# Performance work log

Measured on AMD Instinct MI355X. Metric: run time of the kernel, lower is better.

## Reference

```python
import jax, jax.numpy as jnp
import numpy as np

B, W, L, J, I, O = 512, 1024, 64, 8, 32, 128


def setup_inputs() -> dict:
    key = jax.random.key(0)
    ks = jax.random.split(key, 9)
    wm = jax.random.normal(ks[0], (B, W, L), dtype=jnp.float32)
    constants = jax.random.uniform(ks[1], (J, L), minval=-1.0, maxval=1.0, dtype=jnp.float32)
    gammas = jax.random.uniform(ks[2], (J, L), minval=0.0, maxval=1.0, dtype=jnp.float32)
    body_w = jax.random.normal(ks[3], (J, I, L), dtype=jnp.float32) / np.sqrt(L).astype(np.float32)
    body_b = jax.random.normal(ks[4], (J, I), dtype=jnp.float32) * 0.01
    slot_w = jax.random.normal(ks[5], (J, L * I, L), dtype=jnp.float32) / np.sqrt(L).astype(np.float32)
    slot_b = jax.random.normal(ks[6], (J, L * I), dtype=jnp.float32) * 0.01
    head_w = jax.random.normal(ks[7], (O, I), dtype=jnp.float32) / np.sqrt(I).astype(np.float32)
    head_b = jax.random.normal(ks[8], (O,), dtype=jnp.float32) * 0.01
    return {"working_memory": wm, "constants": constants, "gammas": gammas,
            "body_w": body_w, "body_b": body_b, "slot_w": slot_w, "slot_b": slot_b,
            "head_w": head_w, "head_b": head_b}


def reference(working_memory, constants, gammas, body_w, body_b, slot_w, slot_b, head_w, head_b):
    temperature = 1.0
    g = jnp.clip(gammas, 0.0, 1.0)            # (J,L), torch.clamp equivalent
    w1 = 1.0 - g                               # per-element weight (1-gamma)
    # match_scores[j,b,w] = sum_l w1[j,l] * (c[j,l] - wm[b,w,l])^2, expanded to
    # avoid materializing a (J,B,W,L) intermediate:
    A = jnp.sum(w1 * constants * constants, axis=1)                      # (J,)
    cross = jnp.einsum('jl,bwl->jbw', w1 * constants, working_memory)    # (J,B,W)
    quad = jnp.einsum('jl,bwl->jbw', w1, working_memory * working_memory)
    scores = A[:, None, None] - 2.0 * cross + quad                       # (J,B,W)
    attn = jax.nn.softmax(-scores / temperature, axis=-1)                # (J,B,W)
    best = jnp.einsum('jbw,bwl->jbl', attn, working_memory)              # (J,B,L)
    total_mq = jnp.sum(attn * scores, axis=-1).sum(axis=0)               # (B,)
    # body: per-premise Linear(L->I), scaled by mean clamped gamma
    captured = jnp.einsum('jbl,jil->jbi', best, body_w) + body_b[:, None, :]
    g_avg = g.mean(axis=1)                                               # (J,)
    captured_vars = jnp.einsum('j,jbi->bi', g_avg, captured)             # (B,I)
    # slot selector: per-premise Linear(L -> L*I), softmax over slots,
    # scatter best_props values into slots (the original inner l-loop).
    slot_logits = jnp.einsum('jbl,jkl->jbk', best, slot_w) + slot_b[:, None, :]
    slot_probs = jax.nn.softmax(slot_logits.reshape(J, -1, L, I), axis=-1)
    captured_vars = captured_vars + jnp.einsum('jbli,jbl->bi', slot_probs, best)
    output = captured_vars @ head_w.T + head_b                           # (B,O)
    confidence = jnp.exp(-total_mq)[:, None]                             # (B,1)
    return confidence * output
```

## Files before the change

### kernel.cpp

```cpp
#include <hip/hip_runtime.h>
#include <cstdint>
#include <cstddef>

#define B_ 512
#define W_ 1024
#define L_ 64
#define J_ 8
#define I_ 32
#define O_ 128


typedef const __attribute__((address_space(1))) void* gas_ptr;
typedef __attribute__((address_space(3))) void* las_ptr;

__global__ __launch_bounds__(64) void k0_prep(const float* __restrict__ constants,
    const float* __restrict__ gammas, float* __restrict__ wcg,
    float* __restrict__ w1g, float* __restrict__ Ag)
{
  const int l = threadIdx.x;
  #pragma unroll
  for (int j = 0; j < J_; ++j) {
    float g = gammas[j*L_ + l];
    g = fminf(fmaxf(g, 0.f), 1.f);
    float c = constants[j*L_ + l];
    float w1 = 1.f - g;
    w1g[j*L_ + l] = w1;
    wcg[j*L_ + l] = -2.f * w1 * c;
  }
  if (l < J_) {
    float a = 0.f;
    for (int c = 0; c < L_; ++c) {
      float g = gammas[l*L_ + c];
      g = fminf(fmaxf(g, 0.f), 1.f);
      float cc = constants[l*L_ + c];
      a += (1.f - g) * cc * cc;
    }
    Ag[l] = a;
  }
}

__global__ __launch_bounds__(256, 2) void k12_fused(const float* __restrict__ wm,
    const float* __restrict__ wcg, const float* __restrict__ w1g,
    const float* __restrict__ Ag, float* __restrict__ bpart, float* __restrict__ stats)
{
  __shared__ __align__(16) float xs[3][64 * 64];
  __shared__ __align__(16) float es[J_ * 64];

  const int tid = threadIdx.x;
  const int b = blockIdx.x, h = blockIdx.y;
  const int lane = tid & 63;
  const int wvu = __builtin_amdgcn_readfirstlane(tid >> 6);
  const int j0  = wvu * 2;
  const int lq = tid & 15, wsl = tid >> 4;
  const int wm15 = lane & 15;
  const int rl = lane >> 4, pcg = lane & 15;

  const float* wmb = wm + (size_t)b * (W_*L_) + (size_t)h * (512*L_);

  float accb[J_][4];
  #pragma unroll
  for (int j = 0; j < J_; ++j)
    #pragma unroll
    for (int q = 0; q < 4; ++q) accb[j][q] = 0.f;
  float esum[2] = {0.f, 0.f}, msum[2] = {0.f, 0.f}, m0v[2];

  float* s0 = &xs[0][0];
  float* s1 = &xs[1][0];
  float* s2 = &xs[2][0];

  auto stage = [&](const float* csrc, float* ldst) {
    #pragma unroll
    for (int k = 0; k < 4; ++k) {
      const int grow = wvu*16 + k*4 + rl;
      const int lcg  = pcg ^ (k*4 + rl);
      __builtin_amdgcn_global_load_lds(
          (gas_ptr)(csrc + grow*64 + lcg*4),
          (las_ptr)(ldst + (wvu*16 + k*4)*64), 16, 0, 0);
    }
  };

  stage(wmb,            s0);
  stage(wmb + 64*L_,    s1);
  asm volatile("s_waitcnt vmcnt(4)" ::: "memory");
  __builtin_amdgcn_s_barrier();

  for (int ch = 0; ch < 8; ++ch) {
    const float* xb = s0;

    if (ch < 6)
      stage(wmb + (ch+2) * (64*L_), s2);

    float a10 = 0.f, a11 = 0.f, a20 = 0.f, a21 = 0.f;
    #pragma unroll
    for (int c = 0; c < 16; ++c) {
      const int col = c ^ wm15;
      float4 x = *(const float4*)&xb[lane*64 + col*4];
      float4 xq;
      xq.x = x.x*x.x; xq.y = x.y*x.y; xq.z = x.z*x.z; xq.w = x.w*x.w;
      float4 wc0 = *(const float4*)(wcg + (j0  )*L_ + c*4);
      float4 wc1 = *(const float4*)(wcg + (j0+1)*L_ + c*4);
      float4 w10 = *(const float4*)(w1g + (j0  )*L_ + c*4);
      float4 w11 = *(const float4*)(w1g + (j0+1)*L_ + c*4);
      a10 = fmaf(wc0.x, x.x, a10); a10 = fmaf(wc0.y, x.y, a10);
      a10 = fmaf(wc0.z, x.z, a10); a10 = fmaf(wc0.w, x.w, a10);
      a11 = fmaf(wc1.x, x.x, a11); a11 = fmaf(wc1.y, x.y, a11);
      a11 = fmaf(wc1.z, x.z, a11); a11 = fmaf(wc1.w, x.w, a11);
      a20 = fmaf(w10.x, xq.x, a20); a20 = fmaf(w10.y, xq.y, a20);
      a20 = fmaf(w10.z, xq.z, a20); a20 = fmaf(w10.w, xq.w, a20);
      a21 = fmaf(w11.x, xq.x, a21); a21 = fmaf(w11.y, xq.y, a21);
      a21 = fmaf(w11.z, xq.z, a21); a21 = fmaf(w11.w, xq.w, a21);
    }
    float s0v = Ag[j0]   + a10 + a20;
    float s1v = Ag[j0+1] + a11 + a21;

    if (ch == 0) {
      float mn0 = s0v, mn1 = s1v;
      #pragma unroll
      for (int off = 1; off < 64; off <<= 1) {
        mn0 = fminf(mn0, __shfl_xor(mn0, off));
        mn1 = fminf(mn1, __shfl_xor(mn1, off));
      }
      m0v[0] = mn0; m0v[1] = mn1;
    }

    float e0 = __expf(m0v[0] - s0v);
    float e1 = __expf(m0v[1] - s1v);
    esum[0] += e0; msum[0] = fmaf(e0, s0v, msum[0]);
    esum[1] += e1; msum[1] = fmaf(e1, s1v, msum[1]);
    es[(j0  )*64 + lane] = e0;
    es[(j0+1)*64 + lane] = e1;

    asm volatile("s_waitcnt lgkmcnt(0)" ::: "memory");
    __builtin_amdgcn_s_barrier();

    float4 x4[4];
    #pragma unroll
    for (int t = 0; t < 4; ++t) {
      const int w2 = wsl*4 + t;
      const int col = lq ^ (w2 & 15);
      x4[t] = *(const float4*)&xb[w2*64 + col*4];
    }
    #pragma unroll
    for (int j = 0; j < J_; ++j) {
      float4 e4 = *(const float4*)&es[j*64 + wsl*4];
      accb[j][0] = fmaf(e4.x, x4[0].x, accb[j][0]);
      accb[j][1] = fmaf(e4.x, x4[0].y, accb[j][1]);
      accb[j][2] = fmaf(e4.x, x4[0].z, accb[j][2]);
      accb[j][3] = fmaf(e4.x, x4[0].w, accb[j][3]);
      accb[j][0] = fmaf(e4.y, x4[1].x, accb[j][0]);
      accb[j][1] = fmaf(e4.y, x4[1].y, accb[j][1]);
      accb[j][2] = fmaf(e4.y, x4[1].z, accb[j][2]);
      accb[j][3] = fmaf(e4.y, x4[1].w, accb[j][3]);
      accb[j][0] = fmaf(e4.z, x4[2].x, accb[j][0]);
      accb[j][1] = fmaf(e4.z, x4[2].y, accb[j][1]);
      accb[j][2] = fmaf(e4.z, x4[2].z, accb[j][2]);
      accb[j][3] = fmaf(e4.z, x4[2].w, accb[j][3]);
      accb[j][0] = fmaf(e4.w, x4[3].x, accb[j][0]);
      accb[j][1] = fmaf(e4.w, x4[3].y, accb[j][1]);
      accb[j][2] = fmaf(e4.w, x4[3].z, accb[j][2]);
      accb[j][3] = fmaf(e4.w, x4[3].w, accb[j][3]);
    }

    if (ch < 6)
      asm volatile("s_waitcnt vmcnt(4) lgkmcnt(0)" ::: "memory");
    else
      asm volatile("s_waitcnt vmcnt(0) lgkmcnt(0)" ::: "memory");
    __builtin_amdgcn_s_barrier();

    float* t = s0; s0 = s1; s1 = s2; s2 = t;
  }

  #pragma unroll
  for (int u = 0; u < 2; ++u) {
    float e = esum[u], m = msum[u];
    #pragma unroll
    for (int off = 1; off < 64; off <<= 1) {
      e += __shfl_xor(e, off);
      m += __shfl_xor(m, off);
    }
    if (lane == 0) {
      float* st = stats + (((size_t)h*B_ + b)*J_ + (j0+u))*4;
      st[0] = m0v[u]; st[1] = e; st[2] = m;
    }
  }

  float* xsf = &xs[0][0];
  #pragma unroll
  for (int j = 0; j < J_; ++j)
    *(float4*)&xsf[((wsl*J_ + j)*16 + lq)*4] = *(float4*)accb[j];
  __syncthreads();
  if (tid < J_*16) {
    int j = tid >> 4, q = tid & 15;
    float4 sum = make_float4(0.f, 0.f, 0.f, 0.f);
    #pragma unroll
    for (int s2i = 0; s2i < 16; ++s2i) {
      float4 p = *(const float4*)&xsf[((s2i*J_ + j)*16 + q)*4];
      sum.x += p.x; sum.y += p.y; sum.z += p.z; sum.w += p.w;
    }
    *(float4*)&bpart[(((size_t)h*J_ + j)*B_ + b)*L_ + q*4] = sum;
  }
}

__global__ __launch_bounds__(128) void k2b_combine(const float* __restrict__ bpart,
    const float* __restrict__ stats, float* __restrict__ best, float* __restrict__ conf)
{
  __shared__ float mred[J_];
  const int b = blockIdx.x, tid = threadIdx.x;
  const int j = tid >> 4, q = tid & 15;
  const float* st0 = stats + ((size_t)b*J_ + j)*4;
  const float* st1 = stats + (((size_t)B_ + b)*J_ + j)*4;
  float m0a = st0[0], E0 = st0[1], M0 = st0[2];
  float m0b = st1[0], E1 = st1[1], M1 = st1[2];
  float M = fminf(m0a, m0b);
  float s0 = __expf(M - m0a), s1 = __expf(M - m0b);
  float E = s0*E0 + s1*E1;
  float inv = 1.f / E;
  float4 p0 = *(const float4*)&bpart[((size_t)j*B_ + b)*L_ + q*4];
  float4 p1 = *(const float4*)&bpart[(((size_t)J_ + j)*B_ + b)*L_ + q*4];
  float4 o;
  o.x = (s0*p0.x + s1*p1.x) * inv;
  o.y = (s0*p0.y + s1*p1.y) * inv;
  o.z = (s0*p0.z + s1*p1.z) * inv;
  o.w = (s0*p0.w + s1*p1.w) * inv;
  *(float4*)&best[((size_t)j*B_ + b)*L_ + q*4] = o;
  if (q == 0) mred[j] = (s0*M0 + s1*M1) * inv;
  __syncthreads();
  if (tid == 0) {
    float mq = 0.f;
    #pragma unroll
    for (int jj = 0; jj < J_; ++jj) mq += mred[jj];
    conf[b] = __expf(-mq);
  }
}

__global__ __launch_bounds__(256) void k3_slot(const float* __restrict__ slot_w,
    const float* __restrict__ slot_b, const float* __restrict__ best,
    float* __restrict__ partial)
{
  const int bx = blockIdx.y;
  const int j = bx >> 3, lg = bx & 7;
  const int bc = blockIdx.x;
  const int tid = threadIdx.x;
  const int wv = tid >> 6, lane = tid & 63;
  const int l2 = lane >> 5, i = lane & 31;
  const int l = lg*8 + wv*2 + l2;
  const int r = l*I_ + i;

  const float* swr = slot_w + ((size_t)j*(L_*I_) + r) * L_;
  float sw[L_];
  #pragma unroll
  for (int c = 0; c < 16; ++c) {
    float4 t = ((const float4*)swr)[c];
    sw[c*4+0] = t.x; sw[c*4+1] = t.y; sw[c*4+2] = t.z; sw[c*4+3] = t.w;
  }
  const float sb = slot_b[j*(L_*I_) + r];
  const float* bestj = best + (size_t)j * B_ * L_;
  float* pout = partial + (size_t)bx * (B_*I_);
  const int lidx = lg*8 + wv*2;

  for (int bi = 0; bi < 32; bi += 4) {
    const int b0 = bc*32 + bi;
    const float* bw[4];
    #pragma unroll
    for (int u = 0; u < 4; ++u) bw[u] = bestj + (size_t)(b0+u) * L_;
    float pa[4], pb[4];
    #pragma unroll
    for (int u = 0; u < 4; ++u) { pa[u] = sb; pb[u] = 0.f; }
    #pragma unroll
    for (int c = 0; c < L_; c += 2) {
      #pragma unroll
      for (int u = 0; u < 4; ++u) {
        pa[u] = fmaf(bw[u][c+0], sw[c+0], pa[u]);
        pb[u] = fmaf(bw[u][c+1], sw[c+1], pb[u]);
      }
    }
    float e[4], sm[4];
    #pragma unroll
    for (int u = 0; u < 4; ++u) { e[u] = __expf(pa[u] + pb[u]); sm[u] = e[u]; }
    #pragma unroll
    for (int mask = 16; mask; mask >>= 1)
      #pragma unroll
      for (int u = 0; u < 4; ++u) sm[u] += __shfl_xor(sm[u], mask);
    float cv[4];
    #pragma unroll
    for (int u = 0; u < 4; ++u) {
      float bv = l2 ? bw[u][lidx+1] : bw[u][lidx];
      cv[u] = (e[u] / sm[u]) * bv;
    }
    #pragma unroll
    for (int u = 0; u < 4; ++u) cv[u] += __shfl_xor(cv[u], 32);
    if (l2 == 0) {
      #pragma unroll
      for (int u = 0; u < 4; ++u)
        pout[(size_t)(b0+u)*I_ + i] = cv[u];
    }
  }
}

__global__ __launch_bounds__(128) void k4_head(const float* __restrict__ partial,
    const float* __restrict__ best, const float* __restrict__ gammas,
    const float* __restrict__ body_w, const float* __restrict__ body_b,
    const float* __restrict__ head_w, const float* __restrict__ head_b,
    const float* __restrict__ conf, float* __restrict__ out)
{
  __shared__ float gavg[J_];
  __shared__ float cvred[4][I_];
  __shared__ float cvf[I_];
  const int b = blockIdx.x, tid = threadIdx.x;
  const int i = tid & 31, q = tid >> 5;
  if (tid < J_) {
    float gsum = 0.f;
    for (int l = 0; l < L_; ++l) {
      float g = gammas[tid*L_ + l];
      gsum += fminf(fmaxf(g, 0.f), 1.f);
    }
    gavg[tid] = gsum * (1.f / L_);
  }
  __syncthreads();

  float acc = 0.f;
  for (int s = q; s < 64; s += 4)
    acc += partial[((size_t)s*B_ + b)*I_ + i];

  #pragma unroll
  for (int u = 0; u < 2; ++u) {
    const int j = q + u*4;
    const float* bwv  = best + ((size_t)j*B_ + b)*L_;
    const float* wrow = body_w + (size_t)(j*I_ + i)*L_;
    float d0 = body_b[j*I_ + i], d1 = 0.f, d2 = 0.f, d3 = 0.f;
    #pragma unroll
    for (int c = 0; c < L_; c += 4) {
      d0 = fmaf(bwv[c+0], wrow[c+0], d0);
      d1 = fmaf(bwv[c+1], wrow[c+1], d1);
      d2 = fmaf(bwv[c+2], wrow[c+2], d2);
      d3 = fmaf(bwv[c+3], wrow[c+3], d3);
    }
    acc = fmaf(gavg[j], (d0 + d1) + (d2 + d3), acc);
  }
  cvred[q][i] = acc;
  __syncthreads();
  if (tid < I_)
    cvf[i] = cvred[0][i] + cvred[1][i] + cvred[2][i] + cvred[3][i];
  __syncthreads();
  float oacc = head_b[tid];
  #pragma unroll
  for (int i2 = 0; i2 < I_; ++i2) oacc = fmaf(cvf[i2], head_w[tid*I_ + i2], oacc);
  out[(size_t)b*O_ + tid] = conf[b] * oacc;
}

extern "C" void kernel_launch(void* const* d_in, const int* in_sizes, int n_in,
                              void* d_out, int out_size, void* d_ws, size_t ws_size,
                              hipStream_t stream) {
  const float* wm        = (const float*)d_in[0];
  const float* constants = (const float*)d_in[1];
  const float* gammas    = (const float*)d_in[2];
  const float* body_w    = (const float*)d_in[3];
  const float* body_b    = (const float*)d_in[4];
  const float* slot_w    = (const float*)d_in[5];
  const float* slot_b    = (const float*)d_in[6];
  const float* head_w    = (const float*)d_in[7];
  const float* head_b    = (const float*)d_in[8];
  float* out = (float*)d_out;

  float* ws      = (float*)d_ws;
  float* wcg     = ws;
  float* w1g     = wcg + J_*L_;
  float* Ag      = w1g + J_*L_;
  float* best    = Ag + 16;
  float* conf    = best + (size_t)J_*B_*L_;
  float* partial = conf + B_;
  float* bpart   = partial + (size_t)64*B_*I_;
  float* stats   = bpart + (size_t)2*J_*B_*L_;

  hipLaunchKernelGGL(k0_prep, dim3(1), dim3(64), 0, stream,
                     constants, gammas, wcg, w1g, Ag);
  hipLaunchKernelGGL(k12_fused, dim3(B_, 2), dim3(256), 0, stream,
                     wm, wcg, w1g, Ag, bpart, stats);
  hipLaunchKernelGGL(k2b_combine, dim3(B_), dim3(128), 0, stream,
                     bpart, stats, best, conf);
  hipLaunchKernelGGL(k3_slot, dim3(16, 64), dim3(256), 0, stream,
                     slot_w, slot_b, best, partial);
  hipLaunchKernelGGL(k4_head, dim3(B_), dim3(128), 0, stream,
                     partial, best, gammas, body_w, body_b, head_w, head_b, conf, out);
}
```

Before: 282.9 us.

## Switch to double-buffered LDS staging and factor score FMAs into Horner form

Shrinks the working-memory LDS ring from three buffers to two. The next chunk is now issued into the buffer just consumed, after this wave's LDS reads drain, instead of before compute. The match-score inner loop is rewritten as (w1*x + wc)*x with split accumulators, which drops the separate squaring multiplies. Less LDS per block could help occupancy, but prefetch distance shrinks. With no barrier before the buffer reuse, other waves may still be reading the buffer while it is overwritten.

```diff
diff --git a/kernel.cpp b/kernel.cpp
--- a/kernel.cpp
+++ b/kernel.cpp
@@ -43,7 +43,7 @@
     const float* __restrict__ wcg, const float* __restrict__ w1g,
     const float* __restrict__ Ag, float* __restrict__ bpart, float* __restrict__ stats)
 {
-  __shared__ __align__(16) float xs[3][64 * 64];
+  __shared__ __align__(16) float xs[2][64 * 64];
   __shared__ __align__(16) float es[J_ * 64];
 
   const int tid = threadIdx.x;
@@ -64,10 +64,6 @@
     for (int q = 0; q < 4; ++q) accb[j][q] = 0.f;
   float esum[2] = {0.f, 0.f}, msum[2] = {0.f, 0.f}, m0v[2];
 
-  float* s0 = &xs[0][0];
-  float* s1 = &xs[1][0];
-  float* s2 = &xs[2][0];
-
   auto stage = [&](const float* csrc, float* ldst) {
     #pragma unroll
     for (int k = 0; k < 4; ++k) {
@@ -79,39 +75,35 @@
     }
   };
 
-  stage(wmb,            s0);
-  stage(wmb + 64*L_,    s1);
+  stage(wmb,         &xs[0][0]);
+  stage(wmb + 64*L_, &xs[1][0]);
   asm volatile("s_waitcnt vmcnt(4)" ::: "memory");
   __builtin_amdgcn_s_barrier();
 
   for (int ch = 0; ch < 8; ++ch) {
-    const float* xb = s0;
-
-    if (ch < 6)
-      stage(wmb + (ch+2) * (64*L_), s2);
-
-    float a10 = 0.f, a11 = 0.f, a20 = 0.f, a21 = 0.f;
+    float* xb = &xs[ch & 1][0];
+
+    float s0a = 0.f, s0b = 0.f, s1a = 0.f, s1b = 0.f;
     #pragma unroll
     for (int c = 0; c < 16; ++c) {
       const int col = c ^ wm15;
       float4 x = *(const float4*)&xb[lane*64 + col*4];
-      float4 xq;
-      xq.x = x.x*x.x; xq.y = x.y*x.y; xq.z = x.z*x.z; xq.w = x.w*x.w;
       float4 wc0 = *(const float4*)(wcg + (j0  )*L_ + c*4);
       float4 wc1 = *(const float4*)(wcg + (j0+1)*L_ + c*4);
       float4 w10 = *(const float4*)(w1g + (j0  )*L_ + c*4);
       float4 w11 = *(const float4*)(w1g + (j0+1)*L_ + c*4);
-      a10 = fmaf(wc0.x, x.x, a10); a10 = fmaf(wc0.y, x.y, a10);
-      a10 = fmaf(wc0.z, x.z, a10); a10 = fmaf(wc0.w, x.w, a10);
-      a11 = fmaf(wc1.x, x.x, a11); a11 = fmaf(wc1.y, x.y, a11);
-      a11 = fmaf(wc1.z, x.z, a11); a11 = fmaf(wc1.w, x.w, a11);
-      a20 = fmaf(w10.x, xq.x, a20); a20 = fmaf(w10.y, xq.y, a20);
-      a20 = fmaf(w10.z, xq.z, a20); a20 = fmaf(w10.w, xq.w, a20);
-      a21 = fmaf(w11.x, xq.x, a21); a21 = fmaf(w11.y, xq.y, a21);
-      a21 = fmaf(w11.z, xq.z, a21); a21 = fmaf(w11.w, xq.w, a21);
-    }
-    float s0v = Ag[j0]   + a10 + a20;
-    float s1v = Ag[j0+1] + a11 + a21;
+      float t;
+      t = fmaf(w10.x, x.x, wc0.x); s0a = fmaf(t, x.x, s0a);
+      t = fmaf(w10.y, x.y, wc0.y); s0b = fmaf(t, x.y, s0b);
+      t = fmaf(w10.z, x.z, wc0.z); s0a = fmaf(t, x.z, s0a);
+      t = fmaf(w10.w, x.w, wc0.w); s0b = fmaf(t, x.w, s0b);
+      t = fmaf(w11.x, x.x, wc1.x); s1a = fmaf(t, x.x, s1a);
+      t = fmaf(w11.y, x.y, wc1.y); s1b = fmaf(t, x.y, s1b);
+      t = fmaf(w11.z, x.z, wc1.z); s1a = fmaf(t, x.z, s1a);
+      t = fmaf(w11.w, x.w, wc1.w); s1b = fmaf(t, x.w, s1b);
+    }
+    float s0v = Ag[j0]   + s0a + s0b;
+    float s1v = Ag[j0+1] + s1a + s1b;
 
     if (ch == 0) {
       float mn0 = s0v, mn1 = s1v;
@@ -161,13 +153,16 @@
       accb[j][3] = fmaf(e4.w, x4[3].w, accb[j][3]);
     }
 
+    asm volatile("s_waitcnt lgkmcnt(0)" ::: "memory");
+
     if (ch < 6)
-      asm volatile("s_waitcnt vmcnt(4) lgkmcnt(0)" ::: "memory");
-    else
-      asm volatile("s_waitcnt vmcnt(0) lgkmcnt(0)" ::: "memory");
+      stage(wmb + (ch+2) * (64*L_), xb);
+
+    if (ch < 6)
+      asm volatile("s_waitcnt vmcnt(4)" ::: "memory");
+    else if (ch == 6)
+      asm volatile("s_waitcnt vmcnt(0)" ::: "memory");
     __builtin_amdgcn_s_barrier();
-
-    float* t = s0; s0 = s1; s1 = s2; s2 = t;
   }
 
   #pragma unroll
```

New measurement: 284.7 us. Within noise of the previous version (+0.6%).
